# Kernel optimization log

Measured on AMD Instinct MI355X. Metric: run time of the kernel, lower is better.

Reference implementation:

```python
import jax, jax.numpy as jnp
import numpy as np

DIM = 1024
HEADS = 16
DIM_HEAD = 64
INNER = HEADS * DIM_HEAD  # 1024
SCALE = DIM_HEAD ** -0.5


def setup_inputs() -> dict:
    key = jax.random.key(0)
    k1, k2, k3, k4 = jax.random.split(key, 4)
    B, N = 4, 2048
    x = jax.random.normal(k1, (B, N, DIM), dtype=jnp.float32)
    # Linear weights stored as [in, out] so y = x @ W (+ b)
    W_qkv = jax.random.normal(k2, (DIM, 3 * INNER), dtype=jnp.float32) * (DIM ** -0.5)
    W_out = jax.random.normal(k3, (INNER, DIM), dtype=jnp.float32) * (INNER ** -0.5)
    b_out = jax.random.normal(k4, (DIM,), dtype=jnp.float32) * 0.01
    return {"x": x, "W_qkv": W_qkv, "W_out": W_out, "b_out": b_out}


def reference(x, W_qkv, W_out, b_out):
    B, N, _ = x.shape
    qkv = x @ W_qkv  # [B, N, 3*INNER]
    q, k, v = jnp.split(qkv, 3, axis=-1)
    # [B, N, H, Dh] -> [B, H, N, Dh]
    reshape = lambda t: t.reshape(B, N, HEADS, DIM_HEAD).transpose(0, 2, 1, 3)
    q, k, v = reshape(q), reshape(k), reshape(v)
    dots = jnp.einsum("bhqd,bhkd->bhqk", q, k) * SCALE  # [B,H,N,N]
    attn = jax.nn.softmax(dots, axis=-1)
    out = jnp.einsum("bhqk,bhkd->bhqd", attn, v)  # [B,H,N,Dh]
    out = out.transpose(0, 2, 1, 3).reshape(B, N, INNER)
    return out @ W_out + b_out
```

## Files before the change

### kernel.cpp

```cpp
#include <hip/hip_runtime.h>


typedef _Float16 half8 __attribute__((ext_vector_type(8)));
typedef __fp16 fp16v2 __attribute__((ext_vector_type(2)));
typedef float floatx4 __attribute__((ext_vector_type(4)));
typedef unsigned short u16;

struct __align__(8) U16x4 { u16 x, y, z, w; };

__device__ __forceinline__ u16 f2h(float f) {
  union { _Float16 h; u16 u; } cv;
  cv.h = (_Float16)f;
  return cv.u;
}

__device__ __forceinline__ void g2l16(const void* g, void* l) {
  __builtin_amdgcn_global_load_lds(
      (const __attribute__((address_space(1))) void*)g,
      (__attribute__((address_space(3))) void*)l, 16, 0, 0);
}

__device__ __forceinline__ int swz(int c) { return (c & 3) ^ ((c >> 3) & 3); }
__device__ __forceinline__ int swz8(int s) { return (s & 7) ^ ((s >> 3) & 7); }

__global__ __launch_bounds__(256) void cast_f32_f16(const float* __restrict__ in,
                                                    u16* __restrict__ out) {
  long long base = ((long long)blockIdx.x * 256 + threadIdx.x) * 8;
  float4 a = *(const float4*)(in + base);
  float4 b = *(const float4*)(in + base + 4);
  U16x4 u0 = {f2h(a.x), f2h(a.y), f2h(a.z), f2h(a.w)};
  U16x4 u1 = {f2h(b.x), f2h(b.y), f2h(b.z), f2h(b.w)};
  *(U16x4*)(out + base) = u0;
  *(U16x4*)(out + base + 4) = u1;
}

__global__ __launch_bounds__(256) void transpose_cast(const float* __restrict__ in,
                                                      u16* __restrict__ out,
                                                      int K, int N) {
  __shared__ u16 ls[64][72];
  const int nTK = K >> 6;
  const int tk = blockIdx.x % nTK;
  const int tn = blockIdx.x / nTK;
  const int tid = threadIdx.x;
#pragma unroll
  for (int i = 0; i < 4; ++i) {
    int idx = i * 256 + tid;
    int r = idx >> 4, c4 = (idx & 15) * 4;
    float4 v = *(const float4*)(in + (long long)(tk * 64 + r) * N + tn * 64 + c4);
    ls[r][c4 + 0] = f2h(v.x);
    ls[r][c4 + 1] = f2h(v.y);
    ls[r][c4 + 2] = f2h(v.z);
    ls[r][c4 + 3] = f2h(v.w);
  }
  __syncthreads();
#pragma unroll
  for (int i = 0; i < 4; ++i) {
    int idx = i * 256 + tid;
    int nr = idx >> 4, kc4 = (idx & 15) * 4;
    U16x4 u = {ls[kc4 + 0][nr], ls[kc4 + 1][nr], ls[kc4 + 2][nr], ls[kc4 + 3][nr]};
    *(U16x4*)(out + (long long)(tn * 64 + nr) * K + tk * 64 + kc4) = u;
  }
}

template <int EPI>
__global__ __launch_bounds__(256, 4) void gemm_f16(const u16* __restrict__ A,
                                                   const u16* __restrict__ Bt,
                                                   u16* __restrict__ O0,
                                                   u16* __restrict__ O1,
                                                   u16* __restrict__ O2,
                                                   float* __restrict__ Of,
                                                   const float* __restrict__ bias) {
  __shared__ __attribute__((aligned(16))) u16 lsA[128 * 64];
  __shared__ __attribute__((aligned(16))) u16 lsB[128 * 64];
  const int tid = threadIdx.x;
  const int lane = tid & 63, wave = tid >> 6;
  const int l15 = lane & 15, quad = lane >> 4;
  const int w7 = l15 & 7;
  const int offk0 = ((quad) ^ w7) * 8;
  const int offk1 = ((4 + quad) ^ w7) * 8;
  const int wm = (wave >> 1) * 64, wn = (wave & 1) * 64;
  const int bm = blockIdx.x & 63;
  const int bn = blockIdx.x >> 6;

  const u16* ga[4];
  const u16* gb[4];
#pragma unroll
  for (int i = 0; i < 4; ++i) {
    int s = i * 256 + tid;
    ga[i] = A + (long long)(bm * 128 + (s >> 3)) * 1024 + swz8(s) * 8;
    gb[i] = Bt + (long long)(bn * 128 + (s >> 3)) * 1024 + swz8(s) * 8;
  }

  floatx4 acc[4][4] = {};

  for (int kt = 0; kt < 16; ++kt) {
    const int ko = kt * 64;
#pragma unroll
    for (int i = 0; i < 4; ++i)
      g2l16(ga[i] + ko, lsA + (i * 256 + wave * 64) * 8);
#pragma unroll
    for (int i = 0; i < 4; ++i)
      g2l16(gb[i] + ko, lsB + (i * 256 + wave * 64) * 8);
    __syncthreads();
#pragma unroll
    for (int ks = 0; ks < 2; ++ks) {
      const int off = ks ? offk1 : offk0;
      half8 af[4], bf[4];
#pragma unroll
      for (int mt = 0; mt < 4; ++mt)
        af[mt] = *(const half8*)(lsA + (wm + mt * 16 + l15) * 64 + off);
#pragma unroll
      for (int nt = 0; nt < 4; ++nt)
        bf[nt] = *(const half8*)(lsB + (wn + nt * 16 + l15) * 64 + off);
#pragma unroll
      for (int mt = 0; mt < 4; ++mt)
#pragma unroll
        for (int nt = 0; nt < 4; ++nt)
          acc[mt][nt] = __builtin_amdgcn_mfma_f32_16x16x32_f16(af[mt], bf[nt], acc[mt][nt], 0, 0, 0);
    }
    __syncthreads();
  }

  if (EPI == 0) {
    const float slq = 0.125f * 1.44269504088896f;
#pragma unroll
    for (int mt = 0; mt < 4; ++mt) {
      int gm = bm * 128 + wm + mt * 16 + quad * 4;
      int b = gm >> 11, n0 = gm & 2047;
#pragma unroll
      for (int nt = 0; nt < 4; ++nt) {
        int gc = bn * 128 + wn + nt * 16 + l15;
        int t = gc >> 10, hd = gc & 1023, h = hd >> 6, d = hd & 63;
        long long bh = (long long)(b * 16 + h);
        if (t == 2) {
          U16x4 u = {f2h(acc[mt][nt][0]), f2h(acc[mt][nt][1]),
                     f2h(acc[mt][nt][2]), f2h(acc[mt][nt][3])};
          *(U16x4*)(O2 + (bh * 64 + d) * 2048 + n0) = u;
        } else {
          float s = (t == 0) ? slq : 1.0f;
          u16* dst = (t == 0 ? O0 : O1) + (bh * 2048 + n0) * 64 + d;
#pragma unroll
          for (int r = 0; r < 4; ++r) dst[r * 64] = f2h(acc[mt][nt][r] * s);
        }
      }
    }
  } else {
#pragma unroll
    for (int mt = 0; mt < 4; ++mt) {
      int gm = bm * 128 + wm + mt * 16 + quad * 4;
#pragma unroll
      for (int nt = 0; nt < 4; ++nt) {
        int gc = bn * 128 + wn + nt * 16 + l15;
        float bv = bias[gc];
#pragma unroll
        for (int r = 0; r < 4; ++r)
          Of[(long long)(gm + r) * 1024 + gc] = acc[mt][nt][r] + bv;
      }
    }
  }
}

__global__ __launch_bounds__(256, 4) void attn_flash(const u16* __restrict__ Qh,
                                                     const u16* __restrict__ Kh,
                                                     const u16* __restrict__ Vt,
                                                     u16* __restrict__ Oh) {
  __shared__ __attribute__((aligned(16))) u16 lsK[2 * 2 * 64 * 32];
  __shared__ __attribute__((aligned(16))) u16 lsV[2 * 2 * 64 * 32];
  __shared__ __attribute__((aligned(16))) u16 lsP[4 * 32 * 32];
  const int tid = threadIdx.x;
  const int lane = tid & 63, wave = tid >> 6;
  const int l15 = lane & 15, quad = lane >> 4;
  const int sw = (l15 >> 1) & 3;
  const int qsw8 = (quad ^ sw) * 8;
  const int bh = blockIdx.x & 63, qt = blockIdx.x >> 6;
  const u16* Qb = Qh + ((long long)bh * 2048 + qt * 128) * 64;
  const u16* Kb = Kh + (long long)bh * 2048 * 64;
  const u16* Vb = Vt + (long long)bh * 64 * 2048;
  u16* lsPw = lsP + wave * 1024;

#pragma unroll
  for (int i = 0; i < 4; ++i) {
    int c = i * 256 + tid;
    g2l16(Qb + ((c >> 2) & 127) * 64 + (c >> 9) * 32 + swz(c) * 8,
          lsK + (i * 256 + wave * 64) * 8);
  }
  __syncthreads();
  half8 qb[2][2];
#pragma unroll
  for (int qt2 = 0; qt2 < 2; ++qt2)
#pragma unroll
    for (int ks = 0; ks < 2; ++ks)
      qb[qt2][ks] = *(const half8*)(lsK + ks * 4096 + (wave * 32 + qt2 * 16 + l15) * 32 + qsw8);
  __syncthreads();

#pragma unroll
  for (int i = 0; i < 2; ++i) {
    int c = i * 256 + tid;
    g2l16(Kb + ((c >> 2) & 63) * 64 + (c >> 8) * 32 + swz(c) * 8,
          lsK + (i * 256 + wave * 64) * 8);
    g2l16(Vb + ((c >> 2) & 63) * 2048 + (c >> 8) * 32 + swz(c) * 8,
          lsV + (i * 256 + wave * 64) * 8);
  }

  half8 onesf;
#pragma unroll
  for (int j = 0; j < 8; ++j) onesf[j] = (_Float16)1.0f;

  floatx4 oacc[2][4] = {};
  floatx4 osum[2] = {};

  for (int kt = 0; kt < 32; ++kt) {
    const int cur = kt & 1;
    const u16* bufK = lsK + cur * 4096;
    const u16* bufV = lsV + cur * 4096;
    __syncthreads();
    if (kt < 31) {
      u16* nK = lsK + (1 - cur) * 4096;
      u16* nV = lsV + (1 - cur) * 4096;
#pragma unroll
      for (int i = 0; i < 2; ++i) {
        int c = i * 256 + tid;
        g2l16(Kb + (kt + 1) * 4096 + ((c >> 2) & 63) * 64 + (c >> 8) * 32 + swz(c) * 8,
              nK + (i * 256 + wave * 64) * 8);
        g2l16(Vb + ((c >> 2) & 63) * 2048 + (kt + 1) * 64 + (c >> 8) * 32 + swz(c) * 8,
              nV + (i * 256 + wave * 64) * 8);
      }
    }
#pragma unroll
    for (int ks4 = 0; ks4 < 2; ++ks4) {
      floatx4 sacc[2][2] = {};
#pragma unroll
      for (int ks = 0; ks < 2; ++ks) {
#pragma unroll
        for (int h = 0; h < 2; ++h) {
          half8 kf = *(const half8*)(bufK + ks * 2048 + ((ks4 * 2 + h) * 16 + l15) * 32 + qsw8);
          sacc[h][0] = __builtin_amdgcn_mfma_f32_16x16x32_f16(kf, qb[0][ks], sacc[h][0], 0, 0, 0);
          sacc[h][1] = __builtin_amdgcn_mfma_f32_16x16x32_f16(kf, qb[1][ks], sacc[h][1], 0, 0, 0);
        }
      }
#pragma unroll
      for (int h = 0; h < 2; ++h) {
#pragma unroll
        for (int qt2 = 0; qt2 < 2; ++qt2) {
          float p0 = __builtin_amdgcn_exp2f(sacc[h][qt2][0]);
          float p1 = __builtin_amdgcn_exp2f(sacc[h][qt2][1]);
          float p2 = __builtin_amdgcn_exp2f(sacc[h][qt2][2]);
          float p3 = __builtin_amdgcn_exp2f(sacc[h][qt2][3]);
          union { fp16v2 h2; unsigned u; } lo, hi;
          lo.h2 = __builtin_amdgcn_cvt_pkrtz(p0, p1);
          hi.h2 = __builtin_amdgcn_cvt_pkrtz(p2, p3);
          uint2 pk = {lo.u, hi.u};
          *(uint2*)(lsPw + (qt2 * 16 + l15) * 32 +
                    (((2 * h + (quad >> 1)) ^ sw) * 8) + (quad & 1) * 4) = pk;
        }
      }
      half8 pa0 = *(const half8*)(lsPw + l15 * 32 + qsw8);
      half8 pa1 = *(const half8*)(lsPw + (16 + l15) * 32 + qsw8);
#pragma unroll
      for (int dt = 0; dt < 4; ++dt) {
        half8 vb = *(const half8*)(bufV + ks4 * 2048 + (dt * 16 + l15) * 32 + qsw8);
        oacc[0][dt] = __builtin_amdgcn_mfma_f32_16x16x32_f16(pa0, vb, oacc[0][dt], 0, 0, 0);
        oacc[1][dt] = __builtin_amdgcn_mfma_f32_16x16x32_f16(pa1, vb, oacc[1][dt], 0, 0, 0);
      }
      osum[0] = __builtin_amdgcn_mfma_f32_16x16x32_f16(pa0, onesf, osum[0], 0, 0, 0);
      osum[1] = __builtin_amdgcn_mfma_f32_16x16x32_f16(pa1, onesf, osum[1], 0, 0, 0);
    }
  }

  const int b = bh >> 4, h = bh & 15;
#pragma unroll
  for (int qt2 = 0; qt2 < 2; ++qt2) {
#pragma unroll
    for (int r = 0; r < 4; ++r) {
      float inv = 1.0f / osum[qt2][r];
      int qrow = qt * 128 + wave * 32 + qt2 * 16 + quad * 4 + r;
      long long rowbase = ((long long)b * 2048 + qrow) * 1024 + h * 64;
#pragma unroll
      for (int dt = 0; dt < 4; ++dt)
        Oh[rowbase + dt * 16 + l15] = f2h(oacc[qt2][dt][r] * inv);
    }
  }
}

extern "C" void kernel_launch(void* const* d_in, const int* in_sizes, int n_in,
                              void* d_out, int out_size, void* d_ws, size_t ws_size,
                              hipStream_t stream) {
  const float* x = (const float*)d_in[0];
  const float* Wqkv = (const float*)d_in[1];
  const float* Wout = (const float*)d_in[2];
  const float* bout = (const float*)d_in[3];
  float* out = (float*)d_out;

  char* ws = (char*)d_ws;
  u16* Xh = (u16*)(ws);
  u16* Wqkvt = (u16*)(ws + (16ll << 20));
  u16* Woutt = (u16*)(ws + (22ll << 20));
  u16* Qh = (u16*)(ws + (24ll << 20));
  u16* Kh = (u16*)(ws + (40ll << 20));
  u16* Vt = (u16*)(ws + (56ll << 20));
  u16* Oh = (u16*)(ws + (72ll << 20));

  cast_f32_f16<<<4096, 256, 0, stream>>>(x, Xh);
  transpose_cast<<<16 * 48, 256, 0, stream>>>(Wqkv, Wqkvt, 1024, 3072);
  transpose_cast<<<16 * 16, 256, 0, stream>>>(Wout, Woutt, 1024, 1024);
  gemm_f16<0><<<64 * 24, 256, 0, stream>>>(Xh, Wqkvt, Qh, Kh, Vt, nullptr, nullptr);
  attn_flash<<<1024, 256, 0, stream>>>(Qh, Kh, Vt, Oh);
  gemm_f16<1><<<64 * 8, 256, 0, stream>>>(Oh, Woutt, nullptr, nullptr, nullptr, out, bout);
}
```

Measured before the change: 264.3 us.

## Double per-wave query tile in flash attention to raise K/V reuse

Result: faster. 244.8 us (-7.4%).

```diff
diff --git a/kernel.cpp b/kernel.cpp
--- a/kernel.cpp
+++ b/kernel.cpp
@@ -160,38 +160,45 @@
   }
 }
 
-__global__ __launch_bounds__(256, 4) void attn_flash(const u16* __restrict__ Qh,
+__global__ __launch_bounds__(256, 2) void attn_flash(const u16* __restrict__ Qh,
                                                      const u16* __restrict__ Kh,
                                                      const u16* __restrict__ Vt,
                                                      u16* __restrict__ Oh) {
   __shared__ __attribute__((aligned(16))) u16 lsK[2 * 2 * 64 * 32];
   __shared__ __attribute__((aligned(16))) u16 lsV[2 * 2 * 64 * 32];
-  __shared__ __attribute__((aligned(16))) u16 lsP[4 * 32 * 32];
+  __shared__ __attribute__((aligned(16))) u16 lsP[4 * 64 * 32];
   const int tid = threadIdx.x;
   const int lane = tid & 63, wave = tid >> 6;
   const int l15 = lane & 15, quad = lane >> 4;
   const int sw = (l15 >> 1) & 3;
   const int qsw8 = (quad ^ sw) * 8;
   const int bh = blockIdx.x & 63, qt = blockIdx.x >> 6;
-  const u16* Qb = Qh + ((long long)bh * 2048 + qt * 128) * 64;
+  const u16* Qb = Qh + ((long long)bh * 2048 + qt * 256) * 64;
   const u16* Kb = Kh + (long long)bh * 2048 * 64;
   const u16* Vb = Vt + (long long)bh * 64 * 2048;
-  u16* lsPw = lsP + wave * 1024;
-
-#pragma unroll
-  for (int i = 0; i < 4; ++i) {
-    int c = i * 256 + tid;
-    g2l16(Qb + ((c >> 2) & 127) * 64 + (c >> 9) * 32 + swz(c) * 8,
-          lsK + (i * 256 + wave * 64) * 8);
-  }
-  __syncthreads();
-  half8 qb[2][2];
-#pragma unroll
-  for (int qt2 = 0; qt2 < 2; ++qt2)
-#pragma unroll
-    for (int ks = 0; ks < 2; ++ks)
-      qb[qt2][ks] = *(const half8*)(lsK + ks * 4096 + (wave * 32 + qt2 * 16 + l15) * 32 + qsw8);
-  __syncthreads();
+  u16* lsPw = lsP + wave * 2048;
+
+  half8 qb[4][2];
+#pragma unroll
+  for (int pass = 0; pass < 2; ++pass) {
+#pragma unroll
+    for (int i = 0; i < 4; ++i) {
+      int c = i * 256 + tid;
+      g2l16(Qb + (pass * 128 + ((c >> 2) & 127)) * 64 + (c >> 9) * 32 + swz(c) * 8,
+            lsK + (i * 256 + wave * 64) * 8);
+    }
+    __syncthreads();
+    if ((wave >> 1) == pass) {
+      const int lrow = (wave & 1) * 64;
+#pragma unroll
+      for (int qt2 = 0; qt2 < 4; ++qt2)
+#pragma unroll
+        for (int ks = 0; ks < 2; ++ks)
+          qb[qt2][ks] = *(const half8*)(lsK + ks * 4096 +
+                                        (lrow + qt2 * 16 + l15) * 32 + qsw8);
+    }
+    __syncthreads();
+  }
 
 #pragma unroll
   for (int i = 0; i < 2; ++i) {
@@ -206,8 +213,8 @@
 #pragma unroll
   for (int j = 0; j < 8; ++j) onesf[j] = (_Float16)1.0f;
 
-  floatx4 oacc[2][4] = {};
-  floatx4 osum[2] = {};
+  floatx4 oacc[4][4] = {};
+  floatx4 osum[4] = {};
 
   for (int kt = 0; kt < 32; ++kt) {
     const int cur = kt & 1;
@@ -228,20 +235,21 @@
     }
 #pragma unroll
     for (int ks4 = 0; ks4 < 2; ++ks4) {
-      floatx4 sacc[2][2] = {};
+      floatx4 sacc[2][4] = {};
 #pragma unroll
       for (int ks = 0; ks < 2; ++ks) {
 #pragma unroll
         for (int h = 0; h < 2; ++h) {
           half8 kf = *(const half8*)(bufK + ks * 2048 + ((ks4 * 2 + h) * 16 + l15) * 32 + qsw8);
-          sacc[h][0] = __builtin_amdgcn_mfma_f32_16x16x32_f16(kf, qb[0][ks], sacc[h][0], 0, 0, 0);
-          sacc[h][1] = __builtin_amdgcn_mfma_f32_16x16x32_f16(kf, qb[1][ks], sacc[h][1], 0, 0, 0);
+#pragma unroll
+          for (int qt2 = 0; qt2 < 4; ++qt2)
+            sacc[h][qt2] = __builtin_amdgcn_mfma_f32_16x16x32_f16(kf, qb[qt2][ks], sacc[h][qt2], 0, 0, 0);
         }
       }
 #pragma unroll
       for (int h = 0; h < 2; ++h) {
 #pragma unroll
-        for (int qt2 = 0; qt2 < 2; ++qt2) {
+        for (int qt2 = 0; qt2 < 4; ++qt2) {
           float p0 = __builtin_amdgcn_exp2f(sacc[h][qt2][0]);
           float p1 = __builtin_amdgcn_exp2f(sacc[h][qt2][1]);
           float p2 = __builtin_amdgcn_exp2f(sacc[h][qt2][2]);
@@ -254,26 +262,30 @@
                     (((2 * h + (quad >> 1)) ^ sw) * 8) + (quad & 1) * 4) = pk;
         }
       }
-      half8 pa0 = *(const half8*)(lsPw + l15 * 32 + qsw8);
-      half8 pa1 = *(const half8*)(lsPw + (16 + l15) * 32 + qsw8);
+      half8 pa[4];
+#pragma unroll
+      for (int qt2 = 0; qt2 < 4; ++qt2)
+        pa[qt2] = *(const half8*)(lsPw + (qt2 * 16 + l15) * 32 + qsw8);
 #pragma unroll
       for (int dt = 0; dt < 4; ++dt) {
         half8 vb = *(const half8*)(bufV + ks4 * 2048 + (dt * 16 + l15) * 32 + qsw8);
-        oacc[0][dt] = __builtin_amdgcn_mfma_f32_16x16x32_f16(pa0, vb, oacc[0][dt], 0, 0, 0);
-        oacc[1][dt] = __builtin_amdgcn_mfma_f32_16x16x32_f16(pa1, vb, oacc[1][dt], 0, 0, 0);
-      }
-      osum[0] = __builtin_amdgcn_mfma_f32_16x16x32_f16(pa0, onesf, osum[0], 0, 0, 0);
-      osum[1] = __builtin_amdgcn_mfma_f32_16x16x32_f16(pa1, onesf, osum[1], 0, 0, 0);
+#pragma unroll
+        for (int qt2 = 0; qt2 < 4; ++qt2)
+          oacc[qt2][dt] = __builtin_amdgcn_mfma_f32_16x16x32_f16(pa[qt2], vb, oacc[qt2][dt], 0, 0, 0);
+      }
+#pragma unroll
+      for (int qt2 = 0; qt2 < 4; ++qt2)
+        osum[qt2] = __builtin_amdgcn_mfma_f32_16x16x32_f16(pa[qt2], onesf, osum[qt2], 0, 0, 0);
     }
   }
 
   const int b = bh >> 4, h = bh & 15;
 #pragma unroll
-  for (int qt2 = 0; qt2 < 2; ++qt2) {
+  for (int qt2 = 0; qt2 < 4; ++qt2) {
 #pragma unroll
     for (int r = 0; r < 4; ++r) {
       float inv = 1.0f / osum[qt2][r];
-      int qrow = qt * 128 + wave * 32 + qt2 * 16 + quad * 4 + r;
+      int qrow = qt * 256 + wave * 64 + qt2 * 16 + quad * 4 + r;
       long long rowbase = ((long long)b * 2048 + qrow) * 1024 + h * 64;
 #pragma unroll
       for (int dt = 0; dt < 4; ++dt)
@@ -304,6 +316,6 @@
   transpose_cast<<<16 * 48, 256, 0, stream>>>(Wqkv, Wqkvt, 1024, 3072);
   transpose_cast<<<16 * 16, 256, 0, stream>>>(Wout, Woutt, 1024, 1024);
   gemm_f16<0><<<64 * 24, 256, 0, stream>>>(Xh, Wqkvt, Qh, Kh, Vt, nullptr, nullptr);
-  attn_flash<<<1024, 256, 0, stream>>>(Qh, Kh, Vt, Oh);
+  attn_flash<<<512, 256, 0, stream>>>(Qh, Kh, Vt, Oh);
   gemm_f16<1><<<64 * 8, 256, 0, stream>>>(Oh, Woutt, nullptr, nullptr, nullptr, out, bout);
 }
```
